# Performance work log

Hardware: AMD Instinct MI355X
Metric: run time of the kernel (lower is better)

## Reference

```python
import jax, jax.numpy as jnp
import numpy as np

NUM_GRAPHS = 512  # batch_size (number of segments)


def setup_inputs() -> dict:
    key = jax.random.key(0)
    k1, k2 = jax.random.split(key)
    x = jax.random.normal(k1, (200000, 256), dtype=jnp.float32)
    batch = jnp.sort(jax.random.randint(k2, (200000,), 0, NUM_GRAPHS, dtype=jnp.int64))
    return {"x": x, "batch": batch}


def reference(x, batch):
    # scatter-add node features into per-graph sums: out[g] = sum_{i: batch[i]==g} x[i]
    return jax.ops.segment_sum(x, batch, num_segments=NUM_GRAPHS)
```

## Files before the change

kernel.cpp:

```cpp
#include <hip/hip_runtime.h>


#define FEAT 256
#define WAVES_PER_BLOCK 4
#define NUM_BLOCKS 1024

__global__ __launch_bounds__(256) void GraphAddPooling_39539468927441_kernel(
    const float* __restrict__ x, const int* __restrict__ batch,
    float* __restrict__ out, int n_rows, int rows_per_block)
{
    const int lane = threadIdx.x & 63;
    const int wave = threadIdx.x >> 6;

    const int r0 = blockIdx.x * rows_per_block;
    int r1 = r0 + rows_per_block;
    if (r1 > n_rows) r1 = n_rows;

    const float4* __restrict__ x4 = (const float4*)x;

    float4 acc = make_float4(0.f, 0.f, 0.f, 0.f);
    int cur = -1;

    for (int r = r0 + wave; r < r1; r += WAVES_PER_BLOCK) {
        const int g = batch[r];
        const float4 v = x4[(size_t)r * (FEAT / 4) + lane];
        if (g != cur) {
            if (cur >= 0) {
                float* o = out + (size_t)cur * FEAT + lane * 4;
                atomicAdd(o + 0, acc.x);
                atomicAdd(o + 1, acc.y);
                atomicAdd(o + 2, acc.z);
                atomicAdd(o + 3, acc.w);
            }
            cur = g;
            acc = make_float4(0.f, 0.f, 0.f, 0.f);
        }
        acc.x += v.x; acc.y += v.y; acc.z += v.z; acc.w += v.w;
    }
    if (cur >= 0) {
        float* o = out + (size_t)cur * FEAT + lane * 4;
        atomicAdd(o + 0, acc.x);
        atomicAdd(o + 1, acc.y);
        atomicAdd(o + 2, acc.z);
        atomicAdd(o + 3, acc.w);
    }
}

extern "C" void kernel_launch(void* const* d_in, const int* in_sizes, int n_in,
                              void* d_out, int out_size, void* d_ws, size_t ws_size,
                              hipStream_t stream) {
    const float* x     = (const float*)d_in[0];
    const int*   batch = (const int*)d_in[1];
    float*       out   = (float*)d_out;

    const int n_rows = in_sizes[1];

    hipMemsetAsync(d_out, 0, (size_t)out_size * sizeof(float), stream);

    const int rows_per_block = (n_rows + NUM_BLOCKS - 1) / NUM_BLOCKS;
    GraphAddPooling_39539468927441_kernel<<<NUM_BLOCKS, 256, 0, stream>>>(
        x, batch, out, n_rows, rows_per_block);
}
```

Measured before the change: 290.7 us.

## Compute segment boundaries and assign one block per segment without atomics

Adds a pre-pass kernel that derives segment start offsets from the sorted batch array. The main kernel then launches one block per segment, accumulates rows with four independent float4 accumulators across a 4x-unrolled loop, reduces across waves in shared memory, and writes the result directly. This removes the output memset and all atomic adds, but launches only 512 blocks and adds a second kernel launch, and the per-segment sizes vary.

New measurement: 282.0 us. 1.03x faster.

```diff
diff --git a/kernel.cpp b/kernel.cpp
--- a/kernel.cpp
+++ b/kernel.cpp
@@ -2,47 +2,72 @@
 
 
 #define FEAT 256
-#define WAVES_PER_BLOCK 4
-#define NUM_BLOCKS 1024
+#define F4   (FEAT / 4)
+#define NSEG 512
+
+__global__ void seg_bounds_kernel(const int* __restrict__ batch,
+                                  int* __restrict__ start, int n) {
+    int r = blockIdx.x * blockDim.x + threadIdx.x;
+    if (r >= n) return;
+    int cur = batch[r];
+    if (r == 0) {
+        for (int g = 0; g <= cur; ++g) start[g] = 0;
+    } else {
+        int prev = batch[r - 1];
+        for (int g = prev + 1; g <= cur; ++g) start[g] = r;
+    }
+    if (r == n - 1) {
+        for (int g = cur + 1; g <= NSEG; ++g) start[g] = n;
+    }
+}
 
 __global__ __launch_bounds__(256) void GraphAddPooling_39539468927441_kernel(
-    const float* __restrict__ x, const int* __restrict__ batch,
-    float* __restrict__ out, int n_rows, int rows_per_block)
+    const float* __restrict__ x, const int* __restrict__ start,
+    float* __restrict__ out)
 {
+    const int g    = blockIdx.x;
     const int lane = threadIdx.x & 63;
     const int wave = threadIdx.x >> 6;
 
-    const int r0 = blockIdx.x * rows_per_block;
-    int r1 = r0 + rows_per_block;
-    if (r1 > n_rows) r1 = n_rows;
+    const int r0 = start[g];
+    const int r1 = start[g + 1];
 
     const float4* __restrict__ x4 = (const float4*)x;
 
-    float4 acc = make_float4(0.f, 0.f, 0.f, 0.f);
-    int cur = -1;
+    float4 a0 = make_float4(0.f, 0.f, 0.f, 0.f);
+    float4 a1 = a0, a2 = a0, a3 = a0;
 
-    for (int r = r0 + wave; r < r1; r += WAVES_PER_BLOCK) {
-        const int g = batch[r];
-        const float4 v = x4[(size_t)r * (FEAT / 4) + lane];
-        if (g != cur) {
-            if (cur >= 0) {
-                float* o = out + (size_t)cur * FEAT + lane * 4;
-                atomicAdd(o + 0, acc.x);
-                atomicAdd(o + 1, acc.y);
-                atomicAdd(o + 2, acc.z);
-                atomicAdd(o + 3, acc.w);
-            }
-            cur = g;
-            acc = make_float4(0.f, 0.f, 0.f, 0.f);
-        }
-        acc.x += v.x; acc.y += v.y; acc.z += v.z; acc.w += v.w;
+    int r = r0 + wave;
+    for (; r + 12 < r1; r += 16) {
+        float4 v0 = x4[(size_t)r        * F4 + lane];
+        float4 v1 = x4[(size_t)(r + 4)  * F4 + lane];
+        float4 v2 = x4[(size_t)(r + 8)  * F4 + lane];
+        float4 v3 = x4[(size_t)(r + 12) * F4 + lane];
+        a0.x += v0.x; a0.y += v0.y; a0.z += v0.z; a0.w += v0.w;
+        a1.x += v1.x; a1.y += v1.y; a1.z += v1.z; a1.w += v1.w;
+        a2.x += v2.x; a2.y += v2.y; a2.z += v2.z; a2.w += v2.w;
+        a3.x += v3.x; a3.y += v3.y; a3.z += v3.z; a3.w += v3.w;
     }
-    if (cur >= 0) {
-        float* o = out + (size_t)cur * FEAT + lane * 4;
-        atomicAdd(o + 0, acc.x);
-        atomicAdd(o + 1, acc.y);
-        atomicAdd(o + 2, acc.z);
-        atomicAdd(o + 3, acc.w);
+    for (; r < r1; r += 4) {
+        float4 v = x4[(size_t)r * F4 + lane];
+        a0.x += v.x; a0.y += v.y; a0.z += v.z; a0.w += v.w;
+    }
+    a0.x += a1.x + a2.x + a3.x;
+    a0.y += a1.y + a2.y + a3.y;
+    a0.z += a1.z + a2.z + a3.z;
+    a0.w += a1.w + a2.w + a3.w;
+
+    __shared__ float4 red[4][F4];
+    red[wave][lane] = a0;
+    __syncthreads();
+    if (wave == 0) {
+        float4 s = red[0][lane];
+        float4 b = red[1][lane], c = red[2][lane], d = red[3][lane];
+        s.x += b.x + c.x + d.x;
+        s.y += b.y + c.y + d.y;
+        s.z += b.z + c.z + d.z;
+        s.w += b.w + c.w + d.w;
+        ((float4*)out)[(size_t)g * F4 + lane] = s;
     }
 }
 
@@ -52,12 +77,10 @@
     const float* x     = (const float*)d_in[0];
     const int*   batch = (const int*)d_in[1];
     float*       out   = (float*)d_out;
+    int*         start = (int*)d_ws;
 
     const int n_rows = in_sizes[1];
 
-    hipMemsetAsync(d_out, 0, (size_t)out_size * sizeof(float), stream);
-
-    const int rows_per_block = (n_rows + NUM_BLOCKS - 1) / NUM_BLOCKS;
-    GraphAddPooling_39539468927441_kernel<<<NUM_BLOCKS, 256, 0, stream>>>(
-        x, batch, out, n_rows, rows_per_block);
+    seg_bounds_kernel<<<(n_rows + 255) / 256, 256, 0, stream>>>(batch, start, n_rows);
+    GraphAddPooling_39539468927441_kernel<<<NSEG, 256, 0, stream>>>(x, start, out);
 }
```
